# Performance work log

Hardware: AMD Instinct MI355X
Metric: run time of the kernel (lower is better)

## Reference

```python
import jax, jax.numpy as jnp
import numpy as np

N_IN = 256      # input nodes
L = 8           # layers (topological levels)
M = 4096        # nodes per layer
K = 16          # fan-in per node
B = 1024        # batch of graph evaluations
SCALE = 4.9     # config.SCALE_ACTIVATION (classic NEAT)


def setup_inputs() -> dict:
    key = jax.random.key(0)
    k1, k2, k3 = jax.random.split(key, 3)
    x = jax.random.normal(k1, (B, N_IN), dtype=jnp.float32)
    W = jax.random.normal(k2, (L, M, K), dtype=jnp.float32) * 0.3
    # edge_idx[l] must index nodes strictly before layer l:
    # valid range [0, N_IN + 1 + l*M)  (+1 is the bias node, value 1.0)
    raw = jax.random.randint(k3, (L, M, K), 0, 2**31 - 1, dtype=jnp.int32)
    offsets = (N_IN + 1 + jnp.arange(L, dtype=jnp.int32) * M)[:, None, None]
    edge_idx = raw % offsets
    return {"x": x, "W": W, "edge_idx": edge_idx}


def reference(x, W, edge_idx):
    # values buffer: inputs ++ bias node (constant 1.0) ++ layer outputs
    bias = jnp.ones((x.shape[0], 1), dtype=x.dtype)
    vals = jnp.concatenate([x, bias], axis=1)            # [B, N_IN+1]
    n_layers = W.shape[0]
    for l in range(n_layers):                            # fixed small layer count
        g = vals[:, edge_idx[l]]                         # gather: [B, M, K]
        pre = SCALE * jnp.einsum('bmk,mk->bm', g, W[l])  # per-node 1xK linear
        vals = jnp.concatenate([vals, jax.nn.sigmoid(pre)], axis=1)
    # output nodes = last layer
    return vals[:, -W.shape[1]:]                         # [B, M]
```

## Files before the change

kernel.cpp:

```cpp
#include <hip/hip_runtime.h>
#include <hip/hip_fp16.h>
#include <cstdint>

#define B_SZ   1024
#define N_IN   256
#define NLAY   8
#define M_SZ   4096
#define K_SZ   16
#define NCOLS  (N_IN + 1 + NLAY * M_SZ)
#define SCALE  4.9f
#define TPB    1024

__global__ __launch_bounds__(256)
void sched_pack_kernel(const int* __restrict__ edge_idx,
                       const float* __restrict__ W,
                       uint32_t* __restrict__ packed) {
    __shared__ uint32_t load[4][16][32];

    const int wave = threadIdx.x >> 6;
    const int lane = threadIdx.x & 63;
    const int g    = blockIdx.x * 4 + wave;
    const int l    = g >> 6;
    const int mblk = g & 63;
    const int m    = mblk * 64 + lane;
    const int base = (l * M_SZ + m) * K_SZ;

    int   idxv[16];
    float wv[16];
    const int4*   ip = reinterpret_cast<const int4*>(edge_idx + base);
    const float4* wp = reinterpret_cast<const float4*>(W + base);
    #pragma unroll
    for (int j = 0; j < 4; ++j) {
        int4   ii = ip[j];
        float4 ww = wp[j];
        idxv[4*j+0] = ii.x; idxv[4*j+1] = ii.y; idxv[4*j+2] = ii.z; idxv[4*j+3] = ii.w;
        wv[4*j+0]   = ww.x; wv[4*j+1]   = ww.y; wv[4*j+2]   = ww.z; wv[4*j+3]   = ww.w;
    }

    uint32_t* lw = &load[wave][0][0];
    #pragma unroll
    for (int s = 0; s < 8; ++s) lw[lane + s * 64] = 0;
    __syncthreads();

    uint32_t amask = 0;
    for (int r = 0; r < 16; ++r) {
        const int b = idxv[r] & 31;
        uint32_t bestload = 0xFFFFFFFFu;
        int      best     = 0;
        #pragma unroll
        for (int s = 0; s < 16; ++s) {
            uint32_t ld = load[wave][s][b];
            ld = (amask & (1u << s)) ? 0xFFFFFFFFu : ld;
            if (ld < bestload) { bestload = ld; best = s; }
        }
        amask |= 1u << best;
        __builtin_amdgcn_sched_barrier(0);
        atomicAdd(&load[wave][best][b], 1u);
        __builtin_amdgcn_sched_barrier(0);

        uint32_t p = ((uint32_t)idxv[r] & 0xFFFFu) |
                     ((uint32_t)__half_as_ushort(__float2half_rn(wv[r])) << 16);
        packed[base + best] = p;
    }
}

template <bool PACKED>
__global__ __launch_bounds__(TPB, 4)
void ffn_kernel(const float* __restrict__ x,
                const uint32_t* __restrict__ packed,
                const int* __restrict__ edge_idx,
                const float* __restrict__ W,
                float* __restrict__ out) {
    __shared__ uint32_t vals[NCOLS];

    const int tid = threadIdx.x;
    const int b0  = blockIdx.x * 2;
    const float* __restrict__ x0 = x + (size_t)b0 * N_IN;
    const float* __restrict__ x1 = x0 + N_IN;

    for (int j = tid; j <= N_IN; j += TPB) {
        float v0 = (j < N_IN) ? x0[j] : 1.0f;
        float v1 = (j < N_IN) ? x1[j] : 1.0f;
        __half2 h2 = __floats2half2_rn(v0, v1);
        vals[j] = *reinterpret_cast<uint32_t*>(&h2);
    }
    __syncthreads();

    const int base = N_IN + 1;
    for (int l = 0; l < NLAY; ++l) {
        for (int i = 0; i < M_SZ / TPB; ++i) {
            const int m = tid + i * TPB;
            float acc0 = 0.f, acc1 = 0.f;

            if (PACKED) {
                const uint4* p4 =
                    reinterpret_cast<const uint4*>(packed + (size_t)(l * M_SZ + m) * K_SZ);
                uint4 pw[4];
                #pragma unroll
                for (int j = 0; j < 4; ++j) pw[j] = p4[j];
                #pragma unroll
                for (int j = 0; j < 4; ++j) {
                    uint32_t words[4] = {pw[j].x, pw[j].y, pw[j].z, pw[j].w};
                    #pragma unroll
                    for (int q = 0; q < 4; ++q) {
                        uint32_t p = words[q];
                        uint32_t v = vals[p & 0xFFFFu];
                        float wf = __half2float(__ushort_as_half((unsigned short)(p >> 16)));
                        __half2 h2 = *reinterpret_cast<__half2*>(&v);
                        acc0 = fmaf(__low2float(h2), wf, acc0);
                        acc1 = fmaf(__high2float(h2), wf, acc1);
                    }
                }
            } else {
                const int4*   i4 = reinterpret_cast<const int4*>(edge_idx + (size_t)(l * M_SZ + m) * K_SZ);
                const float4* w4 = reinterpret_cast<const float4*>(W + (size_t)(l * M_SZ + m) * K_SZ);
                #pragma unroll
                for (int j = 0; j < 4; ++j) {
                    int4   ii = i4[j];
                    float4 ww = w4[j];
                    int   idxs[4] = {ii.x, ii.y, ii.z, ii.w};
                    float wts[4]  = {ww.x, ww.y, ww.z, ww.w};
                    #pragma unroll
                    for (int q = 0; q < 4; ++q) {
                        uint32_t v = vals[idxs[q]];
                        __half2 h2 = *reinterpret_cast<__half2*>(&v);
                        acc0 = fmaf(__low2float(h2), wts[q], acc0);
                        acc1 = fmaf(__high2float(h2), wts[q], acc1);
                    }
                }
            }

            float s0 = 1.0f / (1.0f + __expf(-SCALE * acc0));
            float s1 = 1.0f / (1.0f + __expf(-SCALE * acc1));

            if (l < NLAY - 1) {
                __half2 h2 = __floats2half2_rn(s0, s1);
                vals[base + l * M_SZ + m] = *reinterpret_cast<uint32_t*>(&h2);
            } else {
                out[(size_t)b0 * M_SZ + m]       = s0;
                out[(size_t)(b0 + 1) * M_SZ + m] = s1;
            }
        }
        __syncthreads();
    }
}

extern "C" void kernel_launch(void* const* d_in, const int* in_sizes, int n_in,
                              void* d_out, int out_size, void* d_ws, size_t ws_size,
                              hipStream_t stream) {
    const float* x        = (const float*)d_in[0];
    const float* W        = (const float*)d_in[1];
    const int*   edge_idx = (const int*)d_in[2];
    float*       out      = (float*)d_out;

    const int n = NLAY * M_SZ * K_SZ;
    if (ws_size >= (size_t)n * sizeof(uint32_t)) {
        uint32_t* packed = (uint32_t*)d_ws;
        sched_pack_kernel<<<128, 256, 0, stream>>>(edge_idx, W, packed);
        ffn_kernel<true><<<B_SZ / 2, TPB, 0, stream>>>(x, packed, nullptr, nullptr, out);
    } else {
        ffn_kernel<false><<<B_SZ / 2, TPB, 0, stream>>>(x, nullptr, edge_idx, W, out);
    }
}
```

Baseline: 81.15 us.

## Use capacity-bounded bank-balancing edge schedule, fast sigmoid, and trimmed LDS buffer

Measured after the change: 104.2 us. 28.4% more time.

```diff
diff --git a/kernel.cpp b/kernel.cpp
--- a/kernel.cpp
+++ b/kernel.cpp
@@ -7,15 +7,17 @@
 #define NLAY   8
 #define M_SZ   4096
 #define K_SZ   16
-#define NCOLS  (N_IN + 1 + NLAY * M_SZ)
+#define NCOLS_LDS 28932
 #define SCALE  4.9f
 #define TPB    1024
+
+#define NEG_SCALE_LOG2E  (-7.069205700355921f)
 
 __global__ __launch_bounds__(256)
 void sched_pack_kernel(const int* __restrict__ edge_idx,
                        const float* __restrict__ W,
                        uint32_t* __restrict__ packed) {
-    __shared__ uint32_t load[4][16][32];
+    __shared__ uint32_t cnt[4][16][32];
 
     const int wave = threadIdx.x >> 6;
     const int lane = threadIdx.x & 63;
@@ -37,30 +39,38 @@
         wv[4*j+0]   = ww.x; wv[4*j+1]   = ww.y; wv[4*j+2]   = ww.z; wv[4*j+3]   = ww.w;
     }
 
-    uint32_t* lw = &load[wave][0][0];
+    uint32_t* cw = &cnt[wave][0][0];
     #pragma unroll
-    for (int s = 0; s < 8; ++s) lw[lane + s * 64] = 0;
+    for (int s = 0; s < 8; ++s) cw[lane + s * 64] = 0;
     __syncthreads();
 
-    uint32_t amask = 0;
-    for (int r = 0; r < 16; ++r) {
-        const int b = idxv[r] & 31;
-        uint32_t bestload = 0xFFFFFFFFu;
-        int      best     = 0;
-        #pragma unroll
-        for (int s = 0; s < 16; ++s) {
-            uint32_t ld = load[wave][s][b];
-            ld = (amask & (1u << s)) ? 0xFFFFFFFFu : ld;
-            if (ld < bestload) { bestload = ld; best = s; }
+    uint32_t am = 0;
+    uint32_t dm = 0;
+    for (int cap = 2; cap <= 65; ++cap) {
+        if (dm == 0xFFFFu) break;
+        for (int k = 0; k < 16; ++k) {
+            if ((dm >> k) & 1u) continue;
+            const int b = idxv[k] & 31;
+            uint32_t bl = 0xFFFFFFFFu;
+            int      best = 0;
+            #pragma unroll
+            for (int s = 0; s < 16; ++s) {
+                uint32_t c = cnt[wave][s][b];
+                c = ((am >> s) & 1u) ? 0xFFFFFFFFu : c;
+                if (c < bl) { bl = c; best = s; }
+            }
+            if (bl >= (uint32_t)cap) continue;
+            uint32_t old = atomicAdd(&cnt[wave][best][b], 1u);
+            if (old >= (uint32_t)cap) {
+                atomicSub(&cnt[wave][best][b], 1u);
+                continue;
+            }
+            am |= 1u << best;
+            dm |= 1u << k;
+            uint32_t pkw = ((uint32_t)idxv[k] & 0xFFFFu) |
+                           ((uint32_t)__half_as_ushort(__float2half_rn(wv[k])) << 16);
+            packed[base + best] = pkw;
         }
-        amask |= 1u << best;
-        __builtin_amdgcn_sched_barrier(0);
-        atomicAdd(&load[wave][best][b], 1u);
-        __builtin_amdgcn_sched_barrier(0);
-
-        uint32_t p = ((uint32_t)idxv[r] & 0xFFFFu) |
-                     ((uint32_t)__half_as_ushort(__float2half_rn(wv[r])) << 16);
-        packed[base + best] = p;
     }
 }
 
@@ -71,7 +81,7 @@
                 const int* __restrict__ edge_idx,
                 const float* __restrict__ W,
                 float* __restrict__ out) {
-    __shared__ uint32_t vals[NCOLS];
+    __shared__ uint32_t vals[NCOLS_LDS];
 
     const int tid = threadIdx.x;
     const int b0  = blockIdx.x * 2;
@@ -94,7 +104,7 @@
 
             if (PACKED) {
                 const uint4* p4 =
-                    reinterpret_cast<const uint4*>(packed + (size_t)(l * M_SZ + m) * K_SZ);
+                    reinterpret_cast<const uint4*>(packed + ((size_t)l * M_SZ + m) * K_SZ);
                 uint4 pw[4];
                 #pragma unroll
                 for (int j = 0; j < 4; ++j) pw[j] = p4[j];
@@ -107,13 +117,13 @@
                         uint32_t v = vals[p & 0xFFFFu];
                         float wf = __half2float(__ushort_as_half((unsigned short)(p >> 16)));
                         __half2 h2 = *reinterpret_cast<__half2*>(&v);
-                        acc0 = fmaf(__low2float(h2), wf, acc0);
+                        acc0 = fmaf(__low2float(h2),  wf, acc0);
                         acc1 = fmaf(__high2float(h2), wf, acc1);
                     }
                 }
             } else {
-                const int4*   i4 = reinterpret_cast<const int4*>(edge_idx + (size_t)(l * M_SZ + m) * K_SZ);
-                const float4* w4 = reinterpret_cast<const float4*>(W + (size_t)(l * M_SZ + m) * K_SZ);
+                const int4*   i4 = reinterpret_cast<const int4*>(edge_idx + ((size_t)l * M_SZ + m) * K_SZ);
+                const float4* w4 = reinterpret_cast<const float4*>(W + ((size_t)l * M_SZ + m) * K_SZ);
                 #pragma unroll
                 for (int j = 0; j < 4; ++j) {
                     int4   ii = i4[j];
@@ -124,14 +134,16 @@
                     for (int q = 0; q < 4; ++q) {
                         uint32_t v = vals[idxs[q]];
                         __half2 h2 = *reinterpret_cast<__half2*>(&v);
-                        acc0 = fmaf(__low2float(h2), wts[q], acc0);
+                        acc0 = fmaf(__low2float(h2),  wts[q], acc0);
                         acc1 = fmaf(__high2float(h2), wts[q], acc1);
                     }
                 }
             }
 
-            float s0 = 1.0f / (1.0f + __expf(-SCALE * acc0));
-            float s1 = 1.0f / (1.0f + __expf(-SCALE * acc1));
+            float e0 = __builtin_amdgcn_exp2f(NEG_SCALE_LOG2E * acc0);
+            float e1 = __builtin_amdgcn_exp2f(NEG_SCALE_LOG2E * acc1);
+            float s0 = __builtin_amdgcn_rcpf(1.0f + e0);
+            float s1 = __builtin_amdgcn_rcpf(1.0f + e1);
 
             if (l < NLAY - 1) {
                 __half2 h2 = __floats2half2_rn(s0, s1);
```
